# Kernel tuning notes

Measured on AMD Instinct MI355X. Metric: run time of the kernel, lower is better.

## Reference

```python
import jax, jax.numpy as jnp
import numpy as np

TEMPERATURE = 1.0


def setup_inputs() -> dict:
    key = jax.random.key(0)
    k1, k2, k3, k4, k5 = jax.random.split(key, 5)
    B, S, F = 4, 2048, 2048   # batch, seq, in_features
    E, r, O = 8, 16, 2048     # experts, lora rank, out_features
    x = jax.random.normal(k1, (B, S, F), dtype=jnp.float32)
    protos = jax.random.normal(k2, (E, F), dtype=jnp.float32)
    protos = protos / (jnp.linalg.norm(protos, axis=-1, keepdims=True) + 1e-8)  # unit prototypes (top singular vecs)
    A_stack = jax.random.normal(k3, (E, r, F), dtype=jnp.float32) * 0.02
    B_stack = jax.random.normal(k4, (E, O, r), dtype=jnp.float32) * 0.02
    scales = jax.random.uniform(k5, (E,), dtype=jnp.float32)
    return {"x": x, "prototypes": protos, "A_stack": A_stack,
            "B_stack": B_stack, "scales": scales, "top_k": 2}


def reference(x, prototypes, A_stack, B_stack, scales, top_k):
    B, S, F = x.shape
    tok = x.reshape(-1, F)                       # [t, F]
    t = tok.shape[0]
    # 1) |cosine| similarity to prototypes (protos are unit norm)
    sim = jnp.abs(tok @ prototypes.T)            # [t, E]
    # 2) top-k selection, softmax over selected (others -inf)
    top_v, idx = jax.lax.top_k(sim, top_k)       # [t, k]
    full_score = jnp.full(sim.shape, -jnp.inf, dtype=sim.dtype)
    full_score = full_score.at[jnp.arange(t)[:, None], idx].set(top_v)
    coeff = jax.nn.softmax(full_score / TEMPERATURE, axis=1)   # [t, E]
    # 3-5) per-expert LoRA deltas, scaled, then coefficient-weighted sum
    z = jnp.einsum('tf,erf->ter', tok, A_stack)                # [t, E, r]
    y = jnp.einsum('ter,eor->teo', z, B_stack)                 # [t, E, O]
    y = y * scales[None, :, None]
    delta_flat = jnp.einsum('te,teo->to', coeff, y)            # [t, O]
    # 6) dropout is identity in eval mode
    return delta_flat.reshape(B, S, -1)
```

## Files before the change

### kernel.cpp

```cpp
#include <hip/hip_runtime.h>
#include <hip/hip_bf16.h>

typedef unsigned short u16;
typedef __bf16 bf16x8 __attribute__((ext_vector_type(8)));
typedef float f32x4 __attribute__((ext_vector_type(4)));

#define T_TOTAL 8192
#define F_DIM   2048
#define E_NUM   8
#define R_RANK  16
#define ER_DIM  128
#define O_DIM   2048

__device__ __forceinline__ u16 f2bf(float f) {
  return __builtin_bit_cast(u16, (__bf16)f);
}

__global__ __launch_bounds__(256) void prep_kernel(
    const float* __restrict__ A, const float* __restrict__ Bst,
    u16* __restrict__ Abf, u16* __restrict__ BbfT) {
  const int i = blockIdx.x * 256 + threadIdx.x;
  Abf[i] = f2bf(A[i]);
  const int o = i >> 7, er = i & 127, e = er >> 4, j = er & 15;
  BbfT[i] = f2bf(Bst[e * (O_DIM * R_RANK) + o * R_RANK + j]);
}

__global__ __launch_bounds__(256) void gemm1_kernel(
    const float* __restrict__ x, const float* __restrict__ protos,
    const float* __restrict__ scales, const u16* __restrict__ Abf,
    u16* __restrict__ zc) {
  __shared__ u16 xs[16 * 136];
  __shared__ u16 as_[128 * 136];
  __shared__ float pk[8 * 128];
  __shared__ float sim_lds[16][8];
  __shared__ float w_lds[16][8];

  const int tid  = threadIdx.x;
  const int t0   = blockIdx.x * 16;
  const int row  = tid >> 4;
  const int seg  = tid & 15;
  const int lane = tid & 63;
  const int wave = tid >> 6;
  const int g    = lane >> 4;
  const int lm   = lane & 15;

  float sacc[E_NUM];
#pragma unroll
  for (int e = 0; e < E_NUM; ++e) sacc[e] = 0.f;

  const f32x4 z4 = {0.f, 0.f, 0.f, 0.f};
  f32x4 acc[2];
  acc[0] = z4; acc[1] = z4;

  for (int kt = 0; kt < F_DIM / 128; ++kt) {
    const int kb = kt * 128;
    __syncthreads();

    f32x4 xv[2];
    const float* xp = x + (size_t)(t0 + row) * F_DIM + kb + seg * 4;
    xv[0] = *reinterpret_cast<const f32x4*>(xp);
    xv[1] = *reinterpret_cast<const f32x4*>(xp + 64);

    {
      const int pe = tid >> 5;
      const int pj = (tid & 31) * 4;
      *reinterpret_cast<f32x4*>(&pk[pe * 128 + pj]) =
          *reinterpret_cast<const f32x4*>(protos + (size_t)pe * F_DIM + kb + pj);
    }

#pragma unroll
    for (int it = 0; it < 8; ++it) {
      const int c  = it * 256 + tid;
      const int er = c >> 4;
      const int ks = (c & 15) * 8;
      *reinterpret_cast<uint4*>(&as_[er * 136 + ks]) =
          *reinterpret_cast<const uint4*>(Abf + (size_t)er * F_DIM + kb + ks);
    }

#pragma unroll
    for (int p = 0; p < 2; ++p) {
      ushort4 h;
      h.x = f2bf(xv[p][0]); h.y = f2bf(xv[p][1]);
      h.z = f2bf(xv[p][2]); h.w = f2bf(xv[p][3]);
      *reinterpret_cast<ushort4*>(&xs[row * 136 + seg * 4 + p * 64]) = h;
    }
    __syncthreads();

#pragma unroll
    for (int p = 0; p < 2; ++p) {
#pragma unroll
      for (int e = 0; e < E_NUM; ++e) {
        f32x4 pv = *reinterpret_cast<const f32x4*>(&pk[e * 128 + seg * 4 + p * 64]);
        sacc[e] += xv[p][0] * pv[0] + xv[p][1] * pv[1] +
                   xv[p][2] * pv[2] + xv[p][3] * pv[3];
      }
    }

#pragma unroll
    for (int kk = 0; kk < 4; ++kk) {
      bf16x8 av = *reinterpret_cast<const bf16x8*>(&xs[lm * 136 + kk * 32 + g * 8]);
#pragma unroll
      for (int n = 0; n < 2; ++n) {
        bf16x8 bv = *reinterpret_cast<const bf16x8*>(
            &as_[(wave * 32 + n * 16 + lm) * 136 + kk * 32 + g * 8]);
        acc[n] = __builtin_amdgcn_mfma_f32_16x16x32_bf16(av, bv, acc[n], 0, 0, 0);
      }
    }
  }

#pragma unroll
  for (int s = 1; s < 16; s <<= 1)
#pragma unroll
    for (int e = 0; e < E_NUM; ++e)
      sacc[e] += __shfl_xor(sacc[e], s);
  if (seg < E_NUM) sim_lds[row][seg] = sacc[seg];
  __syncthreads();

  if (tid < 16) {
    float sv[E_NUM];
#pragma unroll
    for (int e = 0; e < E_NUM; ++e) sv[e] = fabsf(sim_lds[tid][e]);
    int e0 = 0; float b0 = sv[0];
#pragma unroll
    for (int e = 1; e < E_NUM; ++e) if (sv[e] > b0) { b0 = sv[e]; e0 = e; }
    int e1 = -1; float b1 = -3.0e38f;
#pragma unroll
    for (int e = 0; e < E_NUM; ++e) if (e != e0 && sv[e] > b1) { b1 = sv[e]; e1 = e; }
    const float d  = expf(b1 - b0);
    const float c0 = 1.f / (1.f + d);
    const float c1 = d * c0;
#pragma unroll
    for (int e = 0; e < E_NUM; ++e) w_lds[tid][e] = 0.f;
    w_lds[tid][e0] = c0 * scales[e0];
    w_lds[tid][e1] = c1 * scales[e1];
  }
  __syncthreads();

#pragma unroll
  for (int n = 0; n < 2; ++n) {
    const int er = wave * 32 + n * 16 + lm;
    const int e  = er >> 4;
#pragma unroll
    for (int i = 0; i < 4; ++i) {
      const int tl = g * 4 + i;
      zc[(size_t)(t0 + tl) * ER_DIM + er] = f2bf(acc[n][i] * w_lds[tl][e]);
    }
  }
}

__global__ __launch_bounds__(256) void gemm2_kernel(
    const u16* __restrict__ zc, const u16* __restrict__ BbfT,
    float* __restrict__ out) {
  __shared__ u16 zcs[128 * 136];
  __shared__ u16 bbs[64 * 136];

  const int tid  = threadIdx.x;
  const int o0   = blockIdx.x * 64;
  const int t0   = blockIdx.y * 128;
  const int lane = tid & 63;
  const int wave = tid >> 6;
  const int wm   = wave >> 1;
  const int wn   = wave & 1;
  const int g    = lane >> 4;
  const int lm   = lane & 15;

#pragma unroll
  for (int it = 0; it < 8; ++it) {
    const int c = it * 256 + tid;
    const int r = c >> 4;
    const int ks = (c & 15) * 8;
    *reinterpret_cast<uint4*>(&zcs[r * 136 + ks]) =
        *reinterpret_cast<const uint4*>(zc + (size_t)(t0 + r) * ER_DIM + ks);
  }
#pragma unroll
  for (int it = 0; it < 4; ++it) {
    const int c = it * 256 + tid;
    const int r = c >> 4;
    const int ks = (c & 15) * 8;
    *reinterpret_cast<uint4*>(&bbs[r * 136 + ks]) =
        *reinterpret_cast<const uint4*>(BbfT + (size_t)(o0 + r) * ER_DIM + ks);
  }
  __syncthreads();

  const f32x4 z4 = {0.f, 0.f, 0.f, 0.f};
  f32x4 acc[4][2];
#pragma unroll
  for (int m = 0; m < 4; ++m)
#pragma unroll
    for (int n = 0; n < 2; ++n) acc[m][n] = z4;

#pragma unroll
  for (int kk = 0; kk < 4; ++kk) {
    bf16x8 av[4], bv[2];
#pragma unroll
    for (int m = 0; m < 4; ++m)
      av[m] = *reinterpret_cast<const bf16x8*>(
          &zcs[(wm * 64 + m * 16 + lm) * 136 + kk * 32 + g * 8]);
#pragma unroll
    for (int n = 0; n < 2; ++n)
      bv[n] = *reinterpret_cast<const bf16x8*>(
          &bbs[(wn * 32 + n * 16 + lm) * 136 + kk * 32 + g * 8]);
#pragma unroll
    for (int m = 0; m < 4; ++m)
#pragma unroll
      for (int n = 0; n < 2; ++n)
        acc[m][n] = __builtin_amdgcn_mfma_f32_16x16x32_bf16(av[m], bv[n], acc[m][n], 0, 0, 0);
  }

#pragma unroll
  for (int m = 0; m < 4; ++m) {
#pragma unroll
    for (int n = 0; n < 2; ++n) {
      const int o = o0 + wn * 32 + n * 16 + lm;
#pragma unroll
      for (int i = 0; i < 4; ++i) {
        const int t = t0 + wm * 64 + m * 16 + g * 4 + i;
        out[(size_t)t * O_DIM + o] = acc[m][n][i];
      }
    }
  }
}

extern "C" void kernel_launch(void* const* d_in, const int* in_sizes, int n_in,
                              void* d_out, int out_size, void* d_ws, size_t ws_size,
                              hipStream_t stream) {
  const float* x      = (const float*)d_in[0];
  const float* protos = (const float*)d_in[1];
  const float* A      = (const float*)d_in[2];
  const float* Bst    = (const float*)d_in[3];
  const float* scales = (const float*)d_in[4];

  u16* zcw  = (u16*)d_ws;
  u16* Abf  = zcw + (size_t)T_TOTAL * ER_DIM;
  u16* BbfT = Abf + (size_t)ER_DIM * F_DIM;
  float* out = (float*)d_out;

  prep_kernel<<<(ER_DIM * F_DIM) / 256, 256, 0, stream>>>(A, Bst, Abf, BbfT);
  gemm1_kernel<<<T_TOTAL / 16, 256, 0, stream>>>(x, protos, scales, Abf, zcw);
  gemm2_kernel<<<dim3(O_DIM / 64, T_TOTAL / 128), 256, 0, stream>>>(zcw, BbfT, out);
}
```

Baseline: 175.5 us.

## Double-buffer gemm1 with direct-to-LDS loads, swizzle layouts, widen gemm2 tiles

gemm1 now processes 32 tokens per 512-thread block and double-buffers the A, prototype and x tiles. Global-to-LDS loads are issued for the next K slice while MFMAs run on the current one. Padded LDS rows are replaced by XOR-swizzled layouts, with A, B and zc pre-swizzled in global memory so async loads copy contiguously. gemm2 uses 128x128 output tiles and stages results through LDS for coalesced float4 stores. The changes add LDS pressure and occupancy hints, and the swizzles must match across all three kernels.

```diff
diff --git a/kernel.cpp b/kernel.cpp
--- a/kernel.cpp
+++ b/kernel.cpp
@@ -8,115 +8,143 @@
 #define T_TOTAL 8192
 #define F_DIM   2048
 #define E_NUM   8
-#define R_RANK  16
 #define ER_DIM  128
 #define O_DIM   2048
 
 __device__ __forceinline__ u16 f2bf(float f) {
   return __builtin_bit_cast(u16, (__bf16)f);
+}
+__device__ __forceinline__ unsigned pack2(float a, float b) {
+  return (unsigned)f2bf(a) | ((unsigned)f2bf(b) << 16);
+}
+__device__ __forceinline__ void gld16(void* lds, const void* g) {
+  __builtin_amdgcn_global_load_lds(
+      (const __attribute__((address_space(1))) unsigned int*)g,
+      (__attribute__((address_space(3))) unsigned int*)lds, 16, 0, 0);
 }
 
 __global__ __launch_bounds__(256) void prep_kernel(
     const float* __restrict__ A, const float* __restrict__ Bst,
     u16* __restrict__ Abf, u16* __restrict__ BbfT) {
   const int i = blockIdx.x * 256 + threadIdx.x;
-  Abf[i] = f2bf(A[i]);
-  const int o = i >> 7, er = i & 127, e = er >> 4, j = er & 15;
-  BbfT[i] = f2bf(Bst[e * (O_DIM * R_RANK) + o * R_RANK + j]);
-}
-
-__global__ __launch_bounds__(256) void gemm1_kernel(
+  {
+    const int r = i >> 11, c = i & 2047;
+    Abf[i] = f2bf(A[r * F_DIM + (c ^ ((r & 7) << 3))]);
+  }
+  {
+    const int o = i >> 7, ep = i & 127;
+    const int er = ep ^ ((o & 7) << 3);
+    const int e = er >> 4, j = er & 15;
+    BbfT[i] = f2bf(Bst[e * (O_DIM * 16) + o * 16 + j]);
+  }
+}
+
+__global__ __launch_bounds__(512, 2) void gemm1_kernel(
     const float* __restrict__ x, const float* __restrict__ protos,
     const float* __restrict__ scales, const u16* __restrict__ Abf,
     u16* __restrict__ zc) {
-  __shared__ u16 xs[16 * 136];
-  __shared__ u16 as_[128 * 136];
-  __shared__ float pk[8 * 128];
-  __shared__ float sim_lds[16][8];
-  __shared__ float w_lds[16][8];
+  __shared__ u16  as_[2][128 * 128];
+  __shared__ u16  xs [2][32 * 128];
+  __shared__ float pk[2][8 * 128];
+  __shared__ float sim_lds[32][8];
+  __shared__ float w_lds[32][8];
 
   const int tid  = threadIdx.x;
-  const int t0   = blockIdx.x * 16;
+  const int t0   = blockIdx.x * 32;
   const int row  = tid >> 4;
   const int seg  = tid & 15;
   const int lane = tid & 63;
-  const int wave = tid >> 6;
+  const int w    = tid >> 6;
   const int g    = lane >> 4;
   const int lm   = lane & 15;
 
   float sacc[E_NUM];
 #pragma unroll
   for (int e = 0; e < E_NUM; ++e) sacc[e] = 0.f;
-
   const f32x4 z4 = {0.f, 0.f, 0.f, 0.f};
   f32x4 acc[2];
   acc[0] = z4; acc[1] = z4;
 
+#pragma unroll
+  for (int it = 0; it < 4; ++it) {
+    const int c = it * 512 + tid;
+    const int r = c >> 4, ks = (c & 15) * 8;
+    gld16(&as_[0][c * 8], Abf + (size_t)r * F_DIM + ks);
+  }
+  if (tid < 256)
+    gld16(&pk[0][tid * 4], protos + (size_t)(tid >> 5) * F_DIM + (tid & 31) * 4);
+
+  const float* xrow = x + (size_t)(t0 + row) * F_DIM + seg * 8;
+  f32x4 xv0 = *reinterpret_cast<const f32x4*>(xrow);
+  f32x4 xv1 = *reinterpret_cast<const f32x4*>(xrow + 4);
+  {
+    uint4 hv;
+    hv.x = pack2(xv0[0], xv0[1]); hv.y = pack2(xv0[2], xv0[3]);
+    hv.z = pack2(xv1[0], xv1[1]); hv.w = pack2(xv1[2], xv1[3]);
+    *reinterpret_cast<uint4*>(
+        &xs[0][row * 128 + ((seg * 8) ^ ((row & 7) << 3))]) = hv;
+  }
+
+  int buf = 0;
   for (int kt = 0; kt < F_DIM / 128; ++kt) {
-    const int kb = kt * 128;
     __syncthreads();
 
-    f32x4 xv[2];
-    const float* xp = x + (size_t)(t0 + row) * F_DIM + kb + seg * 4;
-    xv[0] = *reinterpret_cast<const f32x4*>(xp);
-    xv[1] = *reinterpret_cast<const f32x4*>(xp + 64);
-
-    {
-      const int pe = tid >> 5;
-      const int pj = (tid & 31) * 4;
-      *reinterpret_cast<f32x4*>(&pk[pe * 128 + pj]) =
-          *reinterpret_cast<const f32x4*>(protos + (size_t)pe * F_DIM + kb + pj);
-    }
-
-#pragma unroll
-    for (int it = 0; it < 8; ++it) {
-      const int c  = it * 256 + tid;
-      const int er = c >> 4;
-      const int ks = (c & 15) * 8;
-      *reinterpret_cast<uint4*>(&as_[er * 136 + ks]) =
-          *reinterpret_cast<const uint4*>(Abf + (size_t)er * F_DIM + kb + ks);
-    }
-
-#pragma unroll
-    for (int p = 0; p < 2; ++p) {
-      ushort4 h;
-      h.x = f2bf(xv[p][0]); h.y = f2bf(xv[p][1]);
-      h.z = f2bf(xv[p][2]); h.w = f2bf(xv[p][3]);
-      *reinterpret_cast<ushort4*>(&xs[row * 136 + seg * 4 + p * 64]) = h;
-    }
-    __syncthreads();
-
-#pragma unroll
-    for (int p = 0; p < 2; ++p) {
-#pragma unroll
-      for (int e = 0; e < E_NUM; ++e) {
-        f32x4 pv = *reinterpret_cast<const f32x4*>(&pk[e * 128 + seg * 4 + p * 64]);
-        sacc[e] += xv[p][0] * pv[0] + xv[p][1] * pv[1] +
-                   xv[p][2] * pv[2] + xv[p][3] * pv[3];
+    f32x4 xn0, xn1;
+    if (kt < 15) {
+      const int kb = (kt + 1) * 128;
+#pragma unroll
+      for (int it = 0; it < 4; ++it) {
+        const int c = it * 512 + tid;
+        const int r = c >> 4, ks = (c & 15) * 8;
+        gld16(&as_[buf ^ 1][c * 8], Abf + (size_t)r * F_DIM + kb + ks);
       }
+      if (tid < 256)
+        gld16(&pk[buf ^ 1][tid * 4],
+              protos + (size_t)(tid >> 5) * F_DIM + kb + (tid & 31) * 4);
+      xn0 = *reinterpret_cast<const f32x4*>(xrow + kb);
+      xn1 = *reinterpret_cast<const f32x4*>(xrow + kb + 4);
+    }
+
+#pragma unroll
+    for (int e = 0; e < E_NUM; ++e) {
+      f32x4 p0 = *reinterpret_cast<const f32x4*>(&pk[buf][e * 128 + seg * 8]);
+      f32x4 p1 = *reinterpret_cast<const f32x4*>(&pk[buf][e * 128 + seg * 8 + 4]);
+      sacc[e] += xv0[0]*p0[0] + xv0[1]*p0[1] + xv0[2]*p0[2] + xv0[3]*p0[3]
+               + xv1[0]*p1[0] + xv1[1]*p1[1] + xv1[2]*p1[2] + xv1[3]*p1[3];
     }
 
 #pragma unroll
     for (int kk = 0; kk < 4; ++kk) {
-      bf16x8 av = *reinterpret_cast<const bf16x8*>(&xs[lm * 136 + kk * 32 + g * 8]);
-#pragma unroll
-      for (int n = 0; n < 2; ++n) {
-        bf16x8 bv = *reinterpret_cast<const bf16x8*>(
-            &as_[(wave * 32 + n * 16 + lm) * 136 + kk * 32 + g * 8]);
-        acc[n] = __builtin_amdgcn_mfma_f32_16x16x32_bf16(av, bv, acc[n], 0, 0, 0);
+      const int cb = (kk * 32 + g * 8) ^ ((lm & 7) << 3);
+      bf16x8 bv = *reinterpret_cast<const bf16x8*>(
+          &as_[buf][(w * 16 + lm) * 128 + cb]);
+#pragma unroll
+      for (int m = 0; m < 2; ++m) {
+        bf16x8 av = *reinterpret_cast<const bf16x8*>(
+            &xs[buf][(m * 16 + lm) * 128 + cb]);
+        acc[m] = __builtin_amdgcn_mfma_f32_16x16x32_bf16(av, bv, acc[m], 0, 0, 0);
       }
     }
+
+    if (kt < 15) {
+      uint4 hv;
+      hv.x = pack2(xn0[0], xn0[1]); hv.y = pack2(xn0[2], xn0[3]);
+      hv.z = pack2(xn1[0], xn1[1]); hv.w = pack2(xn1[2], xn1[3]);
+      *reinterpret_cast<uint4*>(
+          &xs[buf ^ 1][row * 128 + ((seg * 8) ^ ((row & 7) << 3))]) = hv;
+      xv0 = xn0; xv1 = xn1;
+    }
+    buf ^= 1;
   }
 
 #pragma unroll
   for (int s = 1; s < 16; s <<= 1)
 #pragma unroll
-    for (int e = 0; e < E_NUM; ++e)
-      sacc[e] += __shfl_xor(sacc[e], s);
+    for (int e = 0; e < E_NUM; ++e) sacc[e] += __shfl_xor(sacc[e], s);
   if (seg < E_NUM) sim_lds[row][seg] = sacc[seg];
   __syncthreads();
 
-  if (tid < 16) {
+  if (tid < 32) {
     float sv[E_NUM];
 #pragma unroll
     for (int e = 0; e < E_NUM; ++e) sv[e] = fabsf(sim_lds[tid][e]);
@@ -137,87 +165,89 @@
   __syncthreads();
 
 #pragma unroll
-  for (int n = 0; n < 2; ++n) {
-    const int er = wave * 32 + n * 16 + lm;
-    const int e  = er >> 4;
+  for (int m = 0; m < 2; ++m) {
 #pragma unroll
     for (int i = 0; i < 4; ++i) {
-      const int tl = g * 4 + i;
-      zc[(size_t)(t0 + tl) * ER_DIM + er] = f2bf(acc[n][i] * w_lds[tl][e]);
-    }
-  }
-}
-
-__global__ __launch_bounds__(256) void gemm2_kernel(
+      const int tl = m * 16 + g * 4 + i;
+      const int er = w * 16 + lm;
+      zc[(size_t)(t0 + tl) * ER_DIM + (er ^ ((tl & 7) << 3))] =
+          f2bf(acc[m][i] * w_lds[tl][w]);
+    }
+  }
+}
+
+__global__ __launch_bounds__(256, 2) void gemm2_kernel(
     const u16* __restrict__ zc, const u16* __restrict__ BbfT,
     float* __restrict__ out) {
-  __shared__ u16 zcs[128 * 136];
-  __shared__ u16 bbs[64 * 136];
+  __shared__ char smem[128 * 132 * 4];
+  u16*   zcs = (u16*)smem;
+  u16*   bbs = zcs + 128 * 128;
+  float* ob  = (float*)smem;
 
   const int tid  = threadIdx.x;
-  const int o0   = blockIdx.x * 64;
+  const int o0   = blockIdx.x * 128;
   const int t0   = blockIdx.y * 128;
   const int lane = tid & 63;
-  const int wave = tid >> 6;
-  const int wm   = wave >> 1;
-  const int wn   = wave & 1;
-  const int g    = lane >> 4;
-  const int lm   = lane & 15;
+  const int w    = tid >> 6;
+  const int wm   = w >> 1, wn = w & 1;
+  const int g    = lane >> 4, lm = lane & 15;
 
 #pragma unroll
   for (int it = 0; it < 8; ++it) {
     const int c = it * 256 + tid;
-    const int r = c >> 4;
-    const int ks = (c & 15) * 8;
-    *reinterpret_cast<uint4*>(&zcs[r * 136 + ks]) =
-        *reinterpret_cast<const uint4*>(zc + (size_t)(t0 + r) * ER_DIM + ks);
-  }
-#pragma unroll
-  for (int it = 0; it < 4; ++it) {
+    gld16(&zcs[c * 8], zc + (size_t)t0 * ER_DIM + c * 8);
+  }
+#pragma unroll
+  for (int it = 0; it < 8; ++it) {
     const int c = it * 256 + tid;
-    const int r = c >> 4;
-    const int ks = (c & 15) * 8;
-    *reinterpret_cast<uint4*>(&bbs[r * 136 + ks]) =
-        *reinterpret_cast<const uint4*>(BbfT + (size_t)(o0 + r) * ER_DIM + ks);
+    gld16(&bbs[c * 8], BbfT + (size_t)o0 * ER_DIM + c * 8);
   }
   __syncthreads();
 
   const f32x4 z4 = {0.f, 0.f, 0.f, 0.f};
-  f32x4 acc[4][2];
+  f32x4 acc[4][4];
 #pragma unroll
   for (int m = 0; m < 4; ++m)
 #pragma unroll
-    for (int n = 0; n < 2; ++n) acc[m][n] = z4;
+    for (int n = 0; n < 4; ++n) acc[m][n] = z4;
 
 #pragma unroll
   for (int kk = 0; kk < 4; ++kk) {
-    bf16x8 av[4], bv[2];
+    const int cb = (kk * 32 + g * 8) ^ ((lm & 7) << 3);
+    bf16x8 av[4], bv[4];
 #pragma unroll
     for (int m = 0; m < 4; ++m)
       av[m] = *reinterpret_cast<const bf16x8*>(
-          &zcs[(wm * 64 + m * 16 + lm) * 136 + kk * 32 + g * 8]);
-#pragma unroll
-    for (int n = 0; n < 2; ++n)
+          &zcs[(wm * 64 + m * 16 + lm) * 128 + cb]);
+#pragma unroll
+    for (int n = 0; n < 4; ++n)
       bv[n] = *reinterpret_cast<const bf16x8*>(
-          &bbs[(wn * 32 + n * 16 + lm) * 136 + kk * 32 + g * 8]);
+          &bbs[(wn * 64 + n * 16 + lm) * 128 + cb]);
 #pragma unroll
     for (int m = 0; m < 4; ++m)
 #pragma unroll
-      for (int n = 0; n < 2; ++n)
-        acc[m][n] = __builtin_amdgcn_mfma_f32_16x16x32_bf16(av[m], bv[n], acc[m][n], 0, 0, 0);
-  }
-
-#pragma unroll
-  for (int m = 0; m < 4; ++m) {
-#pragma unroll
-    for (int n = 0; n < 2; ++n) {
-      const int o = o0 + wn * 32 + n * 16 + lm;
-#pragma unroll
-      for (int i = 0; i < 4; ++i) {
-        const int t = t0 + wm * 64 + m * 16 + g * 4 + i;
-        out[(size_t)t * O_DIM + o] = acc[m][n][i];
-      }
-    }
+      for (int n = 0; n < 4; ++n)
+        acc[m][n] = __builtin_amdgcn_mfma_f32_16x16x32_bf16(av[m], bv[n],
+                                                            acc[m][n], 0, 0, 0);
+  }
+  __syncthreads();
+
+#pragma unroll
+  for (int m = 0; m < 4; ++m)
+#pragma unroll
+    for (int n = 0; n < 4; ++n)
+#pragma unroll
+      for (int i = 0; i < 4; ++i)
+        ob[(wm * 64 + m * 16 + g * 4 + i) * 132 + wn * 64 + n * 16 + lm] =
+            acc[m][n][i];
+  __syncthreads();
+
+#pragma unroll
+  for (int j = 0; j < 16; ++j) {
+    const int idx = j * 256 + tid;
+    const int r = idx >> 5, c = idx & 31;
+    f32x4 v = *reinterpret_cast<const f32x4*>(&ob[r * 132 + c * 4]);
+    *reinterpret_cast<f32x4*>(&out[(size_t)(t0 + r) * O_DIM + o0 + c * 4]) = v;
   }
 }
 
@@ -236,6 +266,6 @@
   float* out = (float*)d_out;
 
   prep_kernel<<<(ER_DIM * F_DIM) / 256, 256, 0, stream>>>(A, Bst, Abf, BbfT);
-  gemm1_kernel<<<T_TOTAL / 16, 256, 0, stream>>>(x, protos, scales, Abf, zcw);
-  gemm2_kernel<<<dim3(O_DIM / 64, T_TOTAL / 128), 256, 0, stream>>>(zcw, BbfT, out);
-}
+  gemm1_kernel<<<T_TOTAL / 32, 512, 0, stream>>>(x, protos, scales, Abf, zcw);
+  gemm2_kernel<<<dim3(O_DIM / 128, T_TOTAL / 128), 256, 0, stream>>>(zcw, BbfT, out);
+}
```

After: 142.7 us. 18.7% less time.
